# Kernel optimization log

Hardware: AMD Instinct MI355X
Metric: run time of the kernel (lower is better)

Reference implementation:

```python
import jax, jax.numpy as jnp
import numpy as np

TINY = 1e-15
K_CURV = -1.0
NEG_K = 1.0
SQRT_NEG_K = 1.0
B, D, OUT = 16384, 1024, 4096


def setup_inputs() -> dict:
    key = jax.random.key(0)
    k1, k2, k3 = jax.random.split(key, 3)
    x = jax.random.normal(k1, (B, D), dtype=jnp.float32)
    # PVManifoldMLR.reset_parameters: z ~ N(0, 0.01), r ~ U(-0.001, 0.001)
    z = 0.01 * jax.random.normal(k2, (OUT, D), dtype=jnp.float32)
    r = jax.random.uniform(k3, (OUT, 1), dtype=jnp.float32, minval=-0.001, maxval=0.001)
    bias = jnp.zeros((OUT,), dtype=jnp.float32)
    return {"x": x, "z": z, "r": r, "bias": bias}


def _mlr(x, z, r):
    # PVManifoldMLR.forward (PVNN Thm 5.2 hyperplane distances)
    z_norm = jnp.clip(jnp.linalg.norm(z, axis=-1, keepdims=True), TINY, None)  # [OUT,1]
    sr = jnp.clip(SQRT_NEG_K * r[:, 0], -15.0, 15.0)                            # [OUT]
    cosh_sr = jnp.cosh(sr)
    sinh_sr = jnp.sinh(sr)
    xz = x @ z.T                                                                 # [B,OUT]
    term_A = cosh_sr[None, :] * xz
    x_sq = jnp.sum(x * x, axis=-1, keepdims=True)                                # [B,1]
    beta_inv = jnp.sqrt(1.0 - K_CURV * x_sq)                                     # sqrt(1+|K|x^2)
    term_B = (sinh_sr[None, :] / SQRT_NEG_K) * z_norm.T * beta_inv
    factor_C = SQRT_NEG_K / z_norm.T
    argument = jnp.clip(factor_C * (term_A - term_B), -1e6, 1e6)
    scale = z_norm.T / SQRT_NEG_K
    return scale * jnp.arcsinh(argument)                                         # [B,OUT]


def reference(x, z, r, bias):
    # PVFC: v = MLR(x) + bias; inner_act='none'; y = (1/sqrt(-K)) * sinh(sqrt(-K) * v)
    v = _mlr(x, z, r) + bias[None, :]
    return (1.0 / SQRT_NEG_K) * jnp.sinh(SQRT_NEG_K * v)
```

## Files before the change

### kernel.cpp

```cpp
#include <hip/hip_runtime.h>
#include <stdint.h>
#include <math.h>

#define B_ROWS 16384
#define D_DIM  1024
#define OUT_N  4096

typedef __bf16 bf16x8 __attribute__((ext_vector_type(8)));
typedef float  f32x4  __attribute__((ext_vector_type(4)));

__device__ __forceinline__ unsigned short f2bf(float f) {
  union { float f; uint32_t u; } v; v.f = f;
  uint32_t u = v.u;
  u += 0x7FFFu + ((u >> 16) & 1u);
  return (unsigned short)(u >> 16);
}


__global__ void prep_x_kernel(const float* __restrict__ x,
                              unsigned short* __restrict__ xbf,
                              float* __restrict__ beta) {
  const int row = blockIdx.x;
  const int t = threadIdx.x;
  const float4 v = reinterpret_cast<const float4*>(x + (size_t)row * D_DIM)[t];
  float ssq = v.x * v.x + v.y * v.y + v.z * v.z + v.w * v.w;
  ushort4 h;
  h.x = f2bf(v.x); h.y = f2bf(v.y); h.z = f2bf(v.z); h.w = f2bf(v.w);
  reinterpret_cast<ushort4*>(xbf + (size_t)row * D_DIM)[t] = h;
#pragma unroll
  for (int off = 32; off > 0; off >>= 1) ssq += __shfl_down(ssq, off);
  __shared__ float ws4[4];
  if ((t & 63) == 0) ws4[t >> 6] = ssq;
  __syncthreads();
  if (t == 0) {
    float s = ws4[0] + ws4[1] + ws4[2] + ws4[3];
    beta[row] = sqrtf(1.0f + s);
  }
}

__global__ void prep_z_kernel(const float* __restrict__ z,
                              const float* __restrict__ r,
                              unsigned short* __restrict__ zbf,
                              float4* __restrict__ zp) {
  const int row = blockIdx.x;
  const int t = threadIdx.x;
  const float4 v = reinterpret_cast<const float4*>(z + (size_t)row * D_DIM)[t];
  float ssq = v.x * v.x + v.y * v.y + v.z * v.z + v.w * v.w;
  ushort4 h;
  h.x = f2bf(v.x); h.y = f2bf(v.y); h.z = f2bf(v.z); h.w = f2bf(v.w);
  reinterpret_cast<ushort4*>(zbf + (size_t)row * D_DIM)[t] = h;
#pragma unroll
  for (int off = 32; off > 0; off >>= 1) ssq += __shfl_down(ssq, off);
  __shared__ float ws4[4];
  if ((t & 63) == 0) ws4[t >> 6] = ssq;
  __syncthreads();
  if (t == 0) {
    float s = ws4[0] + ws4[1] + ws4[2] + ws4[3];
    float zn = fmaxf(sqrtf(s), 1e-15f);
    float sr = fminf(fmaxf(r[row], -15.0f), 15.0f);
    float ch = coshf(sr), sh = sinhf(sr);
    zp[row] = make_float4(ch, sh * zn, zn, 1.0f / zn);
  }
}


__device__ __forceinline__ void gload_lds16(const void* g, void* l) {
  __builtin_amdgcn_global_load_lds((__attribute__((address_space(1))) void*)g,
                                   (__attribute__((address_space(3))) void*)l,
                                   16, 0, 0);
}

#define FENCE() asm volatile("" ::: "memory")
#define BARRIER() do { FENCE(); __builtin_amdgcn_s_barrier(); FENCE(); } while (0)
#define WAITVM4() asm volatile("s_waitcnt vmcnt(4)" ::: "memory")
#define WAITVM0() asm volatile("s_waitcnt vmcnt(0)" ::: "memory")

__device__ __forceinline__ float epi(float arg, float zn, float bia) {
  const float LN2   = 0.6931471805599453f;
  const float LOG2E = 1.4426950408889634f;
  float ax = fabsf(arg);
  float s  = __builtin_amdgcn_sqrtf(fmaf(ax, ax, 1.0f));
  float as = __builtin_amdgcn_logf(ax + s) * LN2;
  float v  = fmaf(zn, copysignf(as, arg), bia);
  float e  = __builtin_amdgcn_exp2f(v * LOG2E);
  return 0.5f * (e - __builtin_amdgcn_rcpf(e));
}

__device__ __forceinline__ void stage_half(const unsigned short* __restrict__ src,
                                           int grow0, int k0,
                                           unsigned short* ldsbase,
                                           int wave, int lane) {
#pragma unroll
  for (int j = 0; j < 2; ++j) {
    const int c = wave * 2 + j;
    const int r = c * 8 + (lane >> 3);
    const int col8 = (lane & 7) ^ (lane >> 3);
    gload_lds16(src + (size_t)(grow0 + r) * D_DIM + k0 + col8 * 8,
                ldsbase + c * 512);
  }
}

__device__ __forceinline__ void load_a(bf16x8 a[4][2], const unsigned short* Ab,
                                       int qm, int lrow, int lgrp) {
  const int key = lrow & 7;
#pragma unroll
  for (int mi = 0; mi < 4; ++mi)
#pragma unroll
    for (int ks = 0; ks < 2; ++ks)
      a[mi][ks] = *reinterpret_cast<const bf16x8*>(
          &Ab[(qm * 64 + mi * 16 + lrow) * 64 + ((ks * 4 + lgrp) ^ key) * 8]);
}

__device__ __forceinline__ void load_b(bf16x8 b[2][2], const unsigned short* Bb,
                                       int qn, int lrow, int lgrp) {
  const int key = lrow & 7;
#pragma unroll
  for (int ni = 0; ni < 2; ++ni)
#pragma unroll
    for (int ks = 0; ks < 2; ++ks)
      b[ni][ks] = *reinterpret_cast<const bf16x8*>(
          &Bb[(qn * 32 + ni * 16 + lrow) * 64 + ((ks * 4 + lgrp) ^ key) * 8]);
}

__device__ __forceinline__ void mma_quad(f32x4 acc[8][4], const bf16x8 a[4][2],
                                         const bf16x8 b[2][2], int qm, int qn) {
  __builtin_amdgcn_s_setprio(1);
#pragma unroll
  for (int mi = 0; mi < 4; ++mi)
#pragma unroll
    for (int ni = 0; ni < 2; ++ni)
#pragma unroll
      for (int ks = 0; ks < 2; ++ks)
        acc[qm * 4 + mi][qn * 2 + ni] = __builtin_amdgcn_mfma_f32_16x16x32_bf16(
            a[mi][ks], b[ni][ks], acc[qm * 4 + mi][qn * 2 + ni], 0, 0, 0);
  __builtin_amdgcn_s_setprio(0);
}

__global__ __launch_bounds__(512) void gemm_fused(
    const unsigned short* __restrict__ xbf,
    const unsigned short* __restrict__ zbf,
    const float* __restrict__ beta,
    const float4* __restrict__ zp,
    const float* __restrict__ bias,
    float* __restrict__ out) {
  __shared__ unsigned short lds[65536];

  const int t = threadIdx.x;
  const int lane = t & 63;
  const int wave = t >> 6;
  const int wm = wave >> 2;
  const int wn = wave & 3;
  const int lrow = lane & 15;
  const int lgrp = lane >> 4;

  const int bid = blockIdx.x;
  const int swz = (bid & 7) * 128 + (bid >> 3);
  const int m0 = (swz >> 4) * 256;
  const int n0 = (swz & 15) * 256;

  unsigned short* A0 = lds + wm * 8192;
  unsigned short* A1 = lds + 32768 + wm * 8192;
  unsigned short* B0 = lds + 16384 + (wn >> 1) * 8192 + (wn & 1) * 4096;
  unsigned short* B1 = B0 + 32768;

  f32x4 acc[8][4] = {};
  bf16x8 a[4][2], b0[2][2], b1[2][2];

  stage_half(xbf, m0,       0, lds,                 wave, lane);
  stage_half(xbf, m0 + 128, 0, lds + 8192,          wave, lane);
  stage_half(zbf, n0,       0, lds + 16384,         wave, lane);
  stage_half(zbf, n0 + 128, 0, lds + 16384 + 8192,  wave, lane);
  stage_half(zbf, n0,      64, lds + 32768 + 16384,        wave, lane);
  stage_half(zbf, n0 + 128,64, lds + 32768 + 16384 + 8192, wave, lane);
  WAITVM4();
  BARRIER();

#pragma unroll 1
  for (int i = 0; i < 8; ++i) {
    const int kA1 = (2 * i + 1) * 64;
    const int kT2 = (2 * i + 2) * 64;
    const int kT3 = (2 * i + 3) * 64;
    const bool more = (i < 7);

    load_a(a, A0, 0, lrow, lgrp);
    load_b(b0, B0, 0, lrow, lgrp);
    stage_half(xbf, m0, kA1, lds + 32768, wave, lane);
    BARRIER();
    mma_quad(acc, a, b0, 0, 0);
    BARRIER();
    load_b(b1, B0, 1, lrow, lgrp);
    stage_half(xbf, m0 + 128, kA1, lds + 32768 + 8192, wave, lane);
    BARRIER();
    mma_quad(acc, a, b1, 0, 1);
    BARRIER();
    load_a(a, A0, 1, lrow, lgrp);
    if (more) stage_half(zbf, n0, kT2, lds + 16384, wave, lane);
    BARRIER();
    mma_quad(acc, a, b0, 1, 0);
    BARRIER();
    if (more) stage_half(zbf, n0 + 128, kT2, lds + 16384 + 8192, wave, lane);
    BARRIER();
    mma_quad(acc, a, b1, 1, 1);
    if (more) { WAITVM4(); } else { WAITVM0(); }
    BARRIER();

    load_a(a, A1, 0, lrow, lgrp);
    load_b(b0, B1, 0, lrow, lgrp);
    if (more) stage_half(xbf, m0, kT2, lds, wave, lane);
    BARRIER();
    mma_quad(acc, a, b0, 0, 0);
    BARRIER();
    load_b(b1, B1, 1, lrow, lgrp);
    if (more) stage_half(xbf, m0 + 128, kT2, lds + 8192, wave, lane);
    BARRIER();
    mma_quad(acc, a, b1, 0, 1);
    BARRIER();
    load_a(a, A1, 1, lrow, lgrp);
    if (more) stage_half(zbf, n0, kT3, lds + 32768 + 16384, wave, lane);
    BARRIER();
    mma_quad(acc, a, b0, 1, 0);
    BARRIER();
    if (more) stage_half(zbf, n0 + 128, kT3, lds + 32768 + 16384 + 8192, wave, lane);
    BARRIER();
    mma_quad(acc, a, b1, 1, 1);
    if (more) WAITVM4();
    BARRIER();
  }

  float bt[32];
#pragma unroll
  for (int mi = 0; mi < 8; ++mi)
#pragma unroll
    for (int j = 0; j < 4; ++j)
      bt[mi * 4 + j] = beta[m0 + wm * 128 + mi * 16 + lgrp * 4 + j];

#pragma unroll
  for (int ni = 0; ni < 4; ++ni) {
    const int o = n0 + wn * 64 + ni * 16 + lrow;
    const float4 p = zp[o];
    const float bia = bias[o];
#pragma unroll
    for (int mi = 0; mi < 8; ++mi) {
      const int r0 = m0 + wm * 128 + mi * 16 + lgrp * 4;
#pragma unroll
      for (int j = 0; j < 4; ++j) {
        float arg = (p.x * acc[mi][ni][j] - p.y * bt[mi * 4 + j]) * p.w;
        arg = fminf(fmaxf(arg, -1e6f), 1e6f);
        out[(size_t)(r0 + j) * OUT_N + o] = epi(arg, p.z, bia);
      }
    }
  }
}


extern "C" void kernel_launch(void* const* d_in, const int* in_sizes, int n_in,
                              void* d_out, int out_size, void* d_ws, size_t ws_size,
                              hipStream_t stream) {
  const float* x    = (const float*)d_in[0];
  const float* z    = (const float*)d_in[1];
  const float* r    = (const float*)d_in[2];
  const float* bias = (const float*)d_in[3];
  float* out = (float*)d_out;

  char* ws = (char*)d_ws;
  unsigned short* xbf = (unsigned short*)ws;
  unsigned short* zbf = (unsigned short*)(ws + (size_t)32 * 1024 * 1024);
  float* beta = (float*)(ws + (size_t)40 * 1024 * 1024);
  float4* zp  = (float4*)(ws + (size_t)40 * 1024 * 1024 + 64 * 1024);

  prep_x_kernel<<<dim3(B_ROWS), dim3(256), 0, stream>>>(x, xbf, beta);
  prep_z_kernel<<<dim3(OUT_N), dim3(256), 0, stream>>>(z, r, zbf, zp);
  gemm_fused<<<dim3((B_ROWS / 256) * (OUT_N / 256)), dim3(512), 0, stream>>>(
      xbf, zbf, beta, zp, bias, out);
}
```

Measured before the change: 212.5 us.

## Merge prep kernels, remap tile swizzle per XCD, reorder epilogue stores

Combines the x and z preprocessing kernels into a single launch that branches on block index, removing one kernel launch and its tail. Changes the block-to-tile mapping so each XCD handles a contiguous 8-row group of M tiles across N, aiming for better L2 reuse of x tiles. Restructures the epilogue to loop over rows outer and columns inner, loading beta per row group and keeping per-column params in registers, which may reduce register pressure but changes store ordering.

New measurement: 197.8 us. 1.07x faster.

```diff
diff --git a/kernel.cpp b/kernel.cpp
--- a/kernel.cpp
+++ b/kernel.cpp
@@ -16,50 +16,49 @@
   return (unsigned short)(u >> 16);
 }
 
-
-__global__ void prep_x_kernel(const float* __restrict__ x,
-                              unsigned short* __restrict__ xbf,
-                              float* __restrict__ beta) {
-  const int row = blockIdx.x;
+__global__ void prep_kernel(const float* __restrict__ x,
+                            const float* __restrict__ z,
+                            const float* __restrict__ r,
+                            unsigned short* __restrict__ xbf,
+                            unsigned short* __restrict__ zbf,
+                            float* __restrict__ beta,
+                            float4* __restrict__ zp) {
+  const int b = blockIdx.x;
   const int t = threadIdx.x;
-  const float4 v = reinterpret_cast<const float4*>(x + (size_t)row * D_DIM)[t];
-  float ssq = v.x * v.x + v.y * v.y + v.z * v.z + v.w * v.w;
-  ushort4 h;
-  h.x = f2bf(v.x); h.y = f2bf(v.y); h.z = f2bf(v.z); h.w = f2bf(v.w);
-  reinterpret_cast<ushort4*>(xbf + (size_t)row * D_DIM)[t] = h;
-#pragma unroll
-  for (int off = 32; off > 0; off >>= 1) ssq += __shfl_down(ssq, off);
   __shared__ float ws4[4];
-  if ((t & 63) == 0) ws4[t >> 6] = ssq;
-  __syncthreads();
-  if (t == 0) {
-    float s = ws4[0] + ws4[1] + ws4[2] + ws4[3];
-    beta[row] = sqrtf(1.0f + s);
-  }
-}
-
-__global__ void prep_z_kernel(const float* __restrict__ z,
-                              const float* __restrict__ r,
-                              unsigned short* __restrict__ zbf,
-                              float4* __restrict__ zp) {
-  const int row = blockIdx.x;
-  const int t = threadIdx.x;
-  const float4 v = reinterpret_cast<const float4*>(z + (size_t)row * D_DIM)[t];
-  float ssq = v.x * v.x + v.y * v.y + v.z * v.z + v.w * v.w;
-  ushort4 h;
-  h.x = f2bf(v.x); h.y = f2bf(v.y); h.z = f2bf(v.z); h.w = f2bf(v.w);
-  reinterpret_cast<ushort4*>(zbf + (size_t)row * D_DIM)[t] = h;
-#pragma unroll
-  for (int off = 32; off > 0; off >>= 1) ssq += __shfl_down(ssq, off);
-  __shared__ float ws4[4];
-  if ((t & 63) == 0) ws4[t >> 6] = ssq;
-  __syncthreads();
-  if (t == 0) {
-    float s = ws4[0] + ws4[1] + ws4[2] + ws4[3];
-    float zn = fmaxf(sqrtf(s), 1e-15f);
-    float sr = fminf(fmaxf(r[row], -15.0f), 15.0f);
-    float ch = coshf(sr), sh = sinhf(sr);
-    zp[row] = make_float4(ch, sh * zn, zn, 1.0f / zn);
+  if (b < B_ROWS) {
+    const int row = b;
+    const float4 v = reinterpret_cast<const float4*>(x + (size_t)row * D_DIM)[t];
+    float ssq = v.x * v.x + v.y * v.y + v.z * v.z + v.w * v.w;
+    ushort4 h;
+    h.x = f2bf(v.x); h.y = f2bf(v.y); h.z = f2bf(v.z); h.w = f2bf(v.w);
+    reinterpret_cast<ushort4*>(xbf + (size_t)row * D_DIM)[t] = h;
+#pragma unroll
+    for (int off = 32; off > 0; off >>= 1) ssq += __shfl_down(ssq, off);
+    if ((t & 63) == 0) ws4[t >> 6] = ssq;
+    __syncthreads();
+    if (t == 0) {
+      float s = ws4[0] + ws4[1] + ws4[2] + ws4[3];
+      beta[row] = sqrtf(1.0f + s);
+    }
+  } else {
+    const int row = b - B_ROWS;
+    const float4 v = reinterpret_cast<const float4*>(z + (size_t)row * D_DIM)[t];
+    float ssq = v.x * v.x + v.y * v.y + v.z * v.z + v.w * v.w;
+    ushort4 h;
+    h.x = f2bf(v.x); h.y = f2bf(v.y); h.z = f2bf(v.z); h.w = f2bf(v.w);
+    reinterpret_cast<ushort4*>(zbf + (size_t)row * D_DIM)[t] = h;
+#pragma unroll
+    for (int off = 32; off > 0; off >>= 1) ssq += __shfl_down(ssq, off);
+    if ((t & 63) == 0) ws4[t >> 6] = ssq;
+    __syncthreads();
+    if (t == 0) {
+      float s = ws4[0] + ws4[1] + ws4[2] + ws4[3];
+      float zn = fmaxf(sqrtf(s), 1e-15f);
+      float sr = fminf(fmaxf(r[row], -15.0f), 15.0f);
+      float ch = coshf(sr), sh = sinhf(sr);
+      zp[row] = make_float4(ch, sh * zn, zn, 1.0f / zn);
+    }
   }
 }
 
@@ -154,9 +153,10 @@
   const int lgrp = lane >> 4;
 
   const int bid = blockIdx.x;
-  const int swz = (bid & 7) * 128 + (bid >> 3);
-  const int m0 = (swz >> 4) * 256;
-  const int n0 = (swz & 15) * 256;
+  const int xcd = bid & 7;
+  const int j   = bid >> 3;
+  const int m0 = (xcd * 8 + (j & 7)) * 256;
+  const int n0 = (j >> 3) * 256;
 
   unsigned short* A0 = lds + wm * 8192;
   unsigned short* A1 = lds + 32768 + wm * 8192;
@@ -227,26 +227,30 @@
     BARRIER();
   }
 
-  float bt[32];
-#pragma unroll
-  for (int mi = 0; mi < 8; ++mi)
-#pragma unroll
-    for (int j = 0; j < 4; ++j)
-      bt[mi * 4 + j] = beta[m0 + wm * 128 + mi * 16 + lgrp * 4 + j];
-
+  float4 pq[4];
+  float biaq[4];
 #pragma unroll
   for (int ni = 0; ni < 4; ++ni) {
     const int o = n0 + wn * 64 + ni * 16 + lrow;
-    const float4 p = zp[o];
-    const float bia = bias[o];
-#pragma unroll
-    for (int mi = 0; mi < 8; ++mi) {
-      const int r0 = m0 + wm * 128 + mi * 16 + lgrp * 4;
-#pragma unroll
-      for (int j = 0; j < 4; ++j) {
-        float arg = (p.x * acc[mi][ni][j] - p.y * bt[mi * 4 + j]) * p.w;
+    pq[ni] = zp[o];
+    biaq[ni] = bias[o];
+  }
+  const int ocol0 = n0 + wn * 64 + lrow;
+
+#pragma unroll
+  for (int mi = 0; mi < 8; ++mi) {
+    const int r0 = m0 + wm * 128 + mi * 16 + lgrp * 4;
+    float bt[4];
+#pragma unroll
+    for (int jj = 0; jj < 4; ++jj) bt[jj] = beta[r0 + jj];
+#pragma unroll
+    for (int jj = 0; jj < 4; ++jj) {
+      const size_t rowbase = (size_t)(r0 + jj) * OUT_N + ocol0;
+#pragma unroll
+      for (int ni = 0; ni < 4; ++ni) {
+        float arg = (pq[ni].x * acc[mi][ni][jj] - pq[ni].y * bt[jj]) * pq[ni].w;
         arg = fminf(fmaxf(arg, -1e6f), 1e6f);
-        out[(size_t)(r0 + j) * OUT_N + o] = epi(arg, p.z, bia);
+        out[rowbase + ni * 16] = epi(arg, pq[ni].z, biaq[ni]);
       }
     }
   }
@@ -268,8 +272,7 @@
   float* beta = (float*)(ws + (size_t)40 * 1024 * 1024);
   float4* zp  = (float4*)(ws + (size_t)40 * 1024 * 1024 + 64 * 1024);
 
-  prep_x_kernel<<<dim3(B_ROWS), dim3(256), 0, stream>>>(x, xbf, beta);
-  prep_z_kernel<<<dim3(OUT_N), dim3(256), 0, stream>>>(z, r, zbf, zp);
+  prep_kernel<<<dim3(B_ROWS + OUT_N), dim3(256), 0, stream>>>(x, z, r, xbf, zbf, beta, zp);
   gemm_fused<<<dim3((B_ROWS / 256) * (OUT_N / 256)), dim3(512), 0, stream>>>(
       xbf, zbf, beta, zp, bias, out);
 }
```
